# Optimization experiments

Hardware: AMD Instinct MI355X
Metric: run time of the kernel (lower is better)

The kernel has to match this reference:

```python
import jax, jax.numpy as jnp
import numpy as np
import math

B, L = 512, 32768
NUM_C, NUM_D = 16, 8
RECIPTIVE, STRIDES = 512, 256
EPS = 1e-4


def setup_inputs() -> dict:
    key = jax.random.key(0)
    kx, kw = jax.random.split(key)
    x = jax.random.normal(kx, (B, L), dtype=jnp.float32)
    stdv = 1.0 / math.sqrt(RECIPTIVE)
    weight = jax.random.uniform(kw, (NUM_C, NUM_D, RECIPTIVE), dtype=jnp.float32,
                                minval=-stdv, maxval=stdv)
    return {"x": x, "weight": weight}


def reference(x, weight):
    # x: [B, L], weight: [C, D, R]
    Lx = x.shape[1]
    # sigma = (W W^T + eps I)^{-1} per capsule, [C, D, D]
    wc = jnp.einsum('cdr,cer->cde', weight, weight)
    sigma = jnp.linalg.inv(wc + EPS * jnp.eye(NUM_D, dtype=weight.dtype))
    # circular sliding windows: [W, R] index map (wraparound matches torch.cat branch)
    starts = jnp.arange(0, Lx, STRIDES)
    idx = (starts[:, None] + jnp.arange(RECIPTIVE)[None, :]) % Lx
    windows = x[:, idx]                                   # [B, W, R]
    proj = jnp.einsum('cdr,bwr->bwcd', weight, windows)    # [B, W, C, D]
    q = jnp.einsum('bwcd,cde,bwce->bwc', proj, sigma, proj)  # quadratic form
    return jnp.mean(jnp.sqrt(q), axis=1)                   # [B, C]
```

## Files before the change

kernel.cpp:

```cpp
#include <hip/hip_runtime.h>

#define NUM_C  16
#define NUM_D  8
#define RECEPT 512
#define LROW   32768
#define EPS_V  1e-4f

#define XELEMS 16640
#define XBYTES 33536

typedef __attribute__((ext_vector_type(8))) short short8;
typedef __attribute__((ext_vector_type(4))) float f32x4;

__device__ __forceinline__ unsigned short f2bf(float f) {
    unsigned int u = __builtin_bit_cast(unsigned int, f);
    u += 0x7fffu + ((u >> 16) & 1u);
    return (unsigned short)(u >> 16);
}

__device__ __forceinline__ int xsw(int a) { return a ^ (((a >> 9) & 7) << 4); }

__global__ void prep_kernel(const float* __restrict__ weight,
                            unsigned short* __restrict__ wfrag,
                            float* __restrict__ out) {
    __shared__ float Wc[NUM_D * RECEPT];
    __shared__ float G[NUM_D][NUM_D];
    __shared__ float Lm[NUM_D][NUM_D];
    const int c = blockIdx.x;
    const int t = threadIdx.x;

    out[c * 256 + t] = 0.f;
    out[c * 256 + t + 4096] = 0.f;

    const float4* wsrc4 = reinterpret_cast<const float4*>(
        weight + (size_t)c * NUM_D * RECEPT);
    float4* Wc4 = reinterpret_cast<float4*>(Wc);
    #pragma unroll
    for (int i = 0; i < 4; ++i) Wc4[t + i * 256] = wsrc4[t + i * 256];
    __syncthreads();

    if (t < 64) {
        int d = t >> 3, e = t & 7;
        const float4* wd4 = reinterpret_cast<const float4*>(&Wc[d * RECEPT]);
        const float4* we4 = reinterpret_cast<const float4*>(&Wc[e * RECEPT]);
        float s = 0.f;
        #pragma unroll 4
        for (int r4 = 0; r4 < RECEPT / 4; ++r4) {
            float4 a = wd4[r4], bb = we4[r4];
            s += a.x * bb.x + a.y * bb.y + a.z * bb.z + a.w * bb.w;
        }
        if (d == e) s += EPS_V;
        G[d][e] = s;
    }
    __syncthreads();
    if (t == 0) {
        for (int i = 0; i < NUM_D; ++i) {
            float diag = G[i][i];
            for (int k = 0; k < i; ++k) diag -= Lm[i][k] * Lm[i][k];
            float di = sqrtf(diag);
            Lm[i][i] = di;
            float inv = 1.f / di;
            for (int jj = i + 1; jj < NUM_D; ++jj) {
                float s = G[jj][i];
                for (int k = 0; k < i; ++k) s -= Lm[jj][k] * Lm[i][k];
                Lm[jj][i] = s * inv;
            }
        }
    }
    __syncthreads();
    for (int r = t; r < RECEPT; r += 256) {
        float y[NUM_D];
        for (int d = 0; d < NUM_D; ++d) {
            float s = Wc[d * RECEPT + r];
            for (int k = 0; k < d; ++k) s -= Lm[d][k] * y[k];
            y[d] = s / Lm[d][d];
        }
        const int kk = r >> 5;
        const int g  = (r >> 3) & 3;
        const int j  = r & 7;
        for (int d = 0; d < NUM_D; ++d) {
            int cd = c * NUM_D + d;
            int ntile = cd >> 4;
            int nl = cd & 15;
            int lane = g * 16 + nl;
            int idx = (((ntile * 16 + kk) * 64) + lane) * 8 + j;
            wfrag[idx] = f2bf(y[d]);
        }
    }
}

__global__ __launch_bounds__(256, 4) void main_kernel(
        const float* __restrict__ x,
        const unsigned short* __restrict__ wfrag,
        float* __restrict__ out) {
    __shared__ char lds[XBYTES];
    const int bid = blockIdx.x;
    const int b = bid >> 1;
    const int h = bid & 1;
    const int t = threadIdx.x;
    const int lane = t & 63;
    const int wv = t >> 6;
    const int rl = lane & 15;
    const int gl = lane >> 4;
    const int nt0 = wv * 2;

    const float4* s4   = reinterpret_cast<const float4*>(x + (size_t)b * LROW + h * 16384);
    const float4* row4 = reinterpret_cast<const float4*>(x + (size_t)b * LROW);

    #pragma unroll
    for (int i = 0; i < 16; ++i) {
        int f4 = i * 256 + t;
        float4 v = s4[f4];
        ushort4 hh;
        hh.x = f2bf(v.x); hh.y = f2bf(v.y); hh.z = f2bf(v.z); hh.w = f2bf(v.w);
        *reinterpret_cast<ushort4*>(lds + xsw(f4 * 8)) = hh;
    }
    if (t < 64) {
        float4 v = h ? row4[t] : s4[4096 + t];
        ushort4 hh;
        hh.x = f2bf(v.x); hh.y = f2bf(v.y); hh.z = f2bf(v.z); hh.w = f2bf(v.w);
        *reinterpret_cast<ushort4*>(lds + xsw((4096 + t) * 8)) = hh;
    }
    __syncthreads();

    f32x4 acc[4][2];
    #pragma unroll
    for (int mi = 0; mi < 4; ++mi)
        #pragma unroll
        for (int ni = 0; ni < 2; ++ni)
            acc[mi][ni] = (f32x4){0.f, 0.f, 0.f, 0.f};

    for (int q = 0; q < 4; ++q) {
        short8 bq[4][2];
        #pragma unroll
        for (int kkq = 0; kkq < 4; ++kkq)
            #pragma unroll
            for (int ni = 0; ni < 2; ++ni)
                bq[kkq][ni] = *reinterpret_cast<const short8*>(
                    wfrag + ((size_t)(((nt0 + ni) * 16 + q * 4 + kkq) * 64 + lane)) * 8);

        #pragma unroll
        for (int kkq = 0; kkq < 4; ++kkq) {
            const int kb = (q * 4 + kkq) * 64 + gl * 16;
            short8 af[4];
            #pragma unroll
            for (int mi = 0; mi < 4; ++mi)
                af[mi] = *reinterpret_cast<const short8*>(
                    lds + xsw((mi * 16 + rl) * 512 + kb));
            #pragma unroll
            for (int mi = 0; mi < 4; ++mi) {
                acc[mi][0] = __builtin_amdgcn_mfma_f32_16x16x32_bf16(af[mi], bq[kkq][0], acc[mi][0], 0, 0, 0);
                acc[mi][1] = __builtin_amdgcn_mfma_f32_16x16x32_bf16(af[mi], bq[kkq][1], acc[mi][1], 0, 0, 0);
            }
        }
    }

    #pragma unroll
    for (int ni = 0; ni < 2; ++ni) {
        float s = 0.f;
        #pragma unroll
        for (int mi = 0; mi < 4; ++mi) {
            #pragma unroll
            for (int r = 0; r < 4; ++r) {
                float p = acc[mi][ni][r];
                float qq = p * p;
                qq += __shfl_xor(qq, 1);
                qq += __shfl_xor(qq, 2);
                qq += __shfl_xor(qq, 4);
                s += sqrtf(qq);
            }
        }
        s += __shfl_xor(s, 16);
        s += __shfl_xor(s, 32);
        if (lane < 16 && (lane & 7) == 0) {
            int c = (wv * 32 + ni * 16 + lane) >> 3;
            atomicAdd(&out[b * NUM_C + c], s * (1.0f / 128.0f));
        }
    }
}

extern "C" void kernel_launch(void* const* d_in, const int* in_sizes, int n_in,
                              void* d_out, int out_size, void* d_ws, size_t ws_size,
                              hipStream_t stream) {
    (void)in_sizes; (void)n_in; (void)ws_size; (void)out_size;
    const float* x      = (const float*)d_in[0];
    const float* weight = (const float*)d_in[1];
    float* out = (float*)d_out;
    unsigned short* wfrag = (unsigned short*)d_ws;

    prep_kernel<<<16, 256, 0, stream>>>(weight, wfrag, out);
    main_kernel<<<1024, 256, 0, stream>>>(x, wfrag, out);
}
```

Before: 34.30 us.

## Load x directly into LDS as fp32 and split rows into quarters

The x slice is now copied straight from global memory into LDS with global_load_lds, kept as fp32, and converted to bf16 only when the MFMA fragments are read. This skips the register round trip and the per-element conversion during staging. The grid doubles so each block covers a quarter row of 32 windows, and the loads of the next weight fragments are moved ahead of the sync and between the k loops so they overlap. In exchange, LDS per block stays about the same while each block does half the MFMA work, and the fragment conversion now happens inside the inner loop.

```diff
diff --git a/kernel.cpp b/kernel.cpp
--- a/kernel.cpp
+++ b/kernel.cpp
@@ -1,4 +1,5 @@
 #include <hip/hip_runtime.h>
+#include <hip/hip_bf16.h>
 
 #define NUM_C  16
 #define NUM_D  8
@@ -6,8 +7,8 @@
 #define LROW   32768
 #define EPS_V  1e-4f
 
-#define XELEMS 16640
-#define XBYTES 33536
+#define XCHUNKS 2112
+#define XBYTES  (XCHUNKS * 16)
 
 typedef __attribute__((ext_vector_type(8))) short short8;
 typedef __attribute__((ext_vector_type(4))) float f32x4;
@@ -18,7 +19,16 @@
     return (unsigned short)(u >> 16);
 }
 
-__device__ __forceinline__ int xsw(int a) { return a ^ (((a >> 9) & 7) << 4); }
+__device__ __forceinline__ int bsw(int a) { return a ^ (((a >> 11) & 7) << 4); }
+
+__device__ __forceinline__ short8 cvt8(f32x4 lo, f32x4 hi) {
+    union { short8 s; __hip_bfloat162 h[4]; } u;
+    u.h[0] = __float22bfloat162_rn(make_float2(lo[0], lo[1]));
+    u.h[1] = __float22bfloat162_rn(make_float2(lo[2], lo[3]));
+    u.h[2] = __float22bfloat162_rn(make_float2(hi[0], hi[1]));
+    u.h[3] = __float22bfloat162_rn(make_float2(hi[2], hi[3]));
+    return u.s;
+}
 
 __global__ void prep_kernel(const float* __restrict__ weight,
                             unsigned short* __restrict__ wfrag,
@@ -95,8 +105,8 @@
         float* __restrict__ out) {
     __shared__ char lds[XBYTES];
     const int bid = blockIdx.x;
-    const int b = bid >> 1;
-    const int h = bid & 1;
+    const int b  = bid >> 2;
+    const int qr = bid & 3;
     const int t = threadIdx.x;
     const int lane = t & 63;
     const int wv = t >> 6;
@@ -104,62 +114,78 @@
     const int gl = lane >> 4;
     const int nt0 = wv * 2;
 
-    const float4* s4   = reinterpret_cast<const float4*>(x + (size_t)b * LROW + h * 16384);
-    const float4* row4 = reinterpret_cast<const float4*>(x + (size_t)b * LROW);
-
-    #pragma unroll
-    for (int i = 0; i < 16; ++i) {
-        int f4 = i * 256 + t;
-        float4 v = s4[f4];
-        ushort4 hh;
-        hh.x = f2bf(v.x); hh.y = f2bf(v.y); hh.z = f2bf(v.z); hh.w = f2bf(v.w);
-        *reinterpret_cast<ushort4*>(lds + xsw(f4 * 8)) = hh;
-    }
-    if (t < 64) {
-        float4 v = h ? row4[t] : s4[4096 + t];
-        ushort4 hh;
-        hh.x = f2bf(v.x); hh.y = f2bf(v.y); hh.z = f2bf(v.z); hh.w = f2bf(v.w);
-        *reinterpret_cast<ushort4*>(lds + xsw((4096 + t) * 8)) = hh;
-    }
-    __syncthreads();
-
-    f32x4 acc[4][2];
-    #pragma unroll
-    for (int mi = 0; mi < 4; ++mi)
+    const char* slice = (const char*)(x + (size_t)b * LROW + qr * 8192);
+
+    #pragma unroll
+    for (int i = 0; i < 8; ++i) {
+        const int cb = i * 256 + wv * 64;
+        const int q = cb + lane;
+        const int sq = q ^ ((q >> 7) & 7);
+        __builtin_amdgcn_global_load_lds(
+            (const __attribute__((address_space(1))) unsigned int*)(slice + sq * 16),
+            (__attribute__((address_space(3))) unsigned int*)(lds + cb * 16),
+            16, 0, 0);
+    }
+    if (wv == 0) {
+        const char* tsrc = (qr == 3) ? (const char*)(x + (size_t)b * LROW)
+                                     : slice + 32768;
+        __builtin_amdgcn_global_load_lds(
+            (const __attribute__((address_space(1))) unsigned int*)(tsrc + lane * 16),
+            (__attribute__((address_space(3))) unsigned int*)(lds + 32768),
+            16, 0, 0);
+    }
+
+    f32x4 acc[2][2];
+    #pragma unroll
+    for (int mi = 0; mi < 2; ++mi)
         #pragma unroll
         for (int ni = 0; ni < 2; ++ni)
             acc[mi][ni] = (f32x4){0.f, 0.f, 0.f, 0.f};
 
+    short8 bq[4][2];
+    #pragma unroll
+    for (int kkq = 0; kkq < 4; ++kkq)
+        #pragma unroll
+        for (int ni = 0; ni < 2; ++ni)
+            bq[kkq][ni] = *reinterpret_cast<const short8*>(
+                wfrag + ((size_t)(((nt0 + ni) * 16 + kkq) * 64 + lane)) * 8);
+
+    __syncthreads();
+
+    #pragma unroll
     for (int q = 0; q < 4; ++q) {
-        short8 bq[4][2];
-        #pragma unroll
-        for (int kkq = 0; kkq < 4; ++kkq)
-            #pragma unroll
-            for (int ni = 0; ni < 2; ++ni)
-                bq[kkq][ni] = *reinterpret_cast<const short8*>(
-                    wfrag + ((size_t)(((nt0 + ni) * 16 + q * 4 + kkq) * 64 + lane)) * 8);
-
         #pragma unroll
         for (int kkq = 0; kkq < 4; ++kkq) {
-            const int kb = (q * 4 + kkq) * 64 + gl * 16;
-            short8 af[4];
-            #pragma unroll
-            for (int mi = 0; mi < 4; ++mi)
-                af[mi] = *reinterpret_cast<const short8*>(
-                    lds + xsw((mi * 16 + rl) * 512 + kb));
-            #pragma unroll
-            for (int mi = 0; mi < 4; ++mi) {
+            const int kk = q * 4 + kkq;
+            short8 af[2];
+            #pragma unroll
+            for (int mi = 0; mi < 2; ++mi) {
+                const int a0 = (mi * 16 + rl) * 1024 + kk * 128 + gl * 32;
+                f32x4 lo = *reinterpret_cast<const f32x4*>(lds + bsw(a0));
+                f32x4 hi = *reinterpret_cast<const f32x4*>(lds + bsw(a0 + 16));
+                af[mi] = cvt8(lo, hi);
+            }
+            #pragma unroll
+            for (int mi = 0; mi < 2; ++mi) {
                 acc[mi][0] = __builtin_amdgcn_mfma_f32_16x16x32_bf16(af[mi], bq[kkq][0], acc[mi][0], 0, 0, 0);
                 acc[mi][1] = __builtin_amdgcn_mfma_f32_16x16x32_bf16(af[mi], bq[kkq][1], acc[mi][1], 0, 0, 0);
             }
         }
+        if (q < 3) {
+            #pragma unroll
+            for (int kkq = 0; kkq < 4; ++kkq)
+                #pragma unroll
+                for (int ni = 0; ni < 2; ++ni)
+                    bq[kkq][ni] = *reinterpret_cast<const short8*>(
+                        wfrag + ((size_t)(((nt0 + ni) * 16 + (q + 1) * 4 + kkq) * 64 + lane)) * 8);
+        }
     }
 
     #pragma unroll
     for (int ni = 0; ni < 2; ++ni) {
         float s = 0.f;
         #pragma unroll
-        for (int mi = 0; mi < 4; ++mi) {
+        for (int mi = 0; mi < 2; ++mi) {
             #pragma unroll
             for (int r = 0; r < 4; ++r) {
                 float p = acc[mi][ni][r];
@@ -189,5 +215,5 @@
     unsigned short* wfrag = (unsigned short*)d_ws;
 
     prep_kernel<<<16, 256, 0, stream>>>(weight, wfrag, out);
-    main_kernel<<<1024, 256, 0, stream>>>(x, wfrag, out);
-}
+    main_kernel<<<2048, 256, 0, stream>>>(x, wfrag, out);
+}
```

Result: slower. 39.31 us (+14.6%).
